# Optimization experiments

Measured on AMD Instinct MI355X. Metric: run time of the kernel, lower is better.

## Reference

```python
import jax, jax.numpy as jnp
import numpy as np

TOP_K = 2


def setup_inputs() -> dict:
    key = jax.random.key(0)
    ks = jax.random.split(key, 6)
    B, S, D, F, E = 4, 2048, 1024, 4096, 8
    sd = 1.0 / np.sqrt(D)
    sf = 1.0 / np.sqrt(F)
    return {
        "x": jax.random.normal(ks[0], (B, S, D), dtype=jnp.float32),
        "gate_w": jax.random.normal(ks[1], (D, E), dtype=jnp.float32) * sd,
        "w1": jax.random.normal(ks[2], (E, D, F), dtype=jnp.float32) * sd,
        "b1": jax.random.normal(ks[3], (E, F), dtype=jnp.float32) * 0.01,
        "w2": jax.random.normal(ks[4], (E, F, D), dtype=jnp.float32) * sf,
        "b2": jax.random.normal(ks[5], (E, D), dtype=jnp.float32) * 0.01,
    }


def reference(x, gate_w, w1, b1, w2, b2):
    B, S, D = x.shape
    E = gate_w.shape[1]
    xf = x.reshape(-1, D)                        # [T, D], T = B*S
    T = xf.shape[0]

    # Gating: top-k logits, softmax over the selected k (in fp32, as in torch)
    logits = xf @ gate_w                         # [T, E]
    top_vals, top_idx = jax.lax.top_k(logits, TOP_K)            # [T, K]
    wts = jax.nn.softmax(top_vals.astype(jnp.float32), axis=-1).astype(x.dtype)

    # Dense combine weights: combine[t, e] = sum_k wts[t,k] * [top_idx[t,k]==e]
    rows = jnp.arange(T)[:, None]
    combine = jnp.zeros((T, E), dtype=x.dtype).at[rows, top_idx].add(wts)

    # Expert FFNs (dropout is identity in eval; torch GELU default = exact erf)
    out = jnp.zeros_like(xf)
    for e in range(E):
        h = jax.nn.gelu(xf @ w1[e] + b1[e], approximate=False)  # [T, F]
        out = out + combine[:, e:e + 1] * (h @ w2[e] + b2[e])
    return out.reshape(B, S, D)
```

## Files before the change

### kernel.cpp

```cpp
#include <hip/hip_runtime.h>


#define T_TOK 8192
#define D_DIM 1024
#define F_DIM 4096
#define E_NUM 8
#define BM 128
#define BN 128
#define BK 32
#define NK1 (D_DIM / BK)
#define NK2 (F_DIM / BK)
#define MAX_TILES (T_TOK * 2 / BM + E_NUM)

typedef float f32x4 __attribute__((ext_vector_type(4)));
typedef short bf16x8 __attribute__((ext_vector_type(8)));

__device__ __forceinline__ unsigned short f2bf(float f) {
  union { float f; unsigned u; } v; v.f = f;
  unsigned r = v.u + 0x7FFFu + ((v.u >> 16) & 1u);
  return (unsigned short)(r >> 16);
}

__device__ __forceinline__ void async_cp16(const unsigned short* g, unsigned short* l) {
  __builtin_amdgcn_global_load_lds((__attribute__((address_space(1))) void*)g,
                                   (__attribute__((address_space(3))) void*)l,
                                   16, 0, 0);
}

#define WAIT_VM2 asm volatile("s_waitcnt vmcnt(2)" ::: "memory")
#define WAIT_LGKM0 asm volatile("s_waitcnt lgkmcnt(0)" ::: "memory")
#define RAW_BARRIER asm volatile("s_barrier" ::: "memory")


__global__ void cast_x_kernel(const float* __restrict__ src,
                              unsigned short* __restrict__ dst, int n4) {
  int i = blockIdx.x * blockDim.x + threadIdx.x;
  if (i >= n4) return;
  float4 v = ((const float4*)src)[i];
  ushort4 o;
  o.x = f2bf(v.x); o.y = f2bf(v.y); o.z = f2bf(v.z); o.w = f2bf(v.w);
  ((ushort4*)dst)[i] = o;
}

__global__ __launch_bounds__(256) void transpose_cast_kernel(
    const float* __restrict__ src, unsigned short* __restrict__ dst,
    int R, int C) {
  __shared__ float tile[64][65];
  int e = blockIdx.z;
  src += (size_t)e * R * C;
  dst += (size_t)e * R * C;
  int c0 = blockIdx.x * 64;
  int r0 = blockIdx.y * 64;
  int t = threadIdx.x;
  int cl = (t & 15) * 4, rl = t >> 4;
#pragma unroll
  for (int i = 0; i < 4; ++i) {
    int r = rl + i * 16;
    float4 v = *(const float4*)(src + (size_t)(r0 + r) * C + c0 + cl);
    tile[r][cl + 0] = v.x;
    tile[r][cl + 1] = v.y;
    tile[r][cl + 2] = v.z;
    tile[r][cl + 3] = v.w;
  }
  __syncthreads();
  int rl2 = (t & 15) * 4, cl2 = t >> 4;
#pragma unroll
  for (int i = 0; i < 4; ++i) {
    int c = cl2 + i * 16;
    ushort4 o;
    o.x = f2bf(tile[rl2 + 0][c]);
    o.y = f2bf(tile[rl2 + 1][c]);
    o.z = f2bf(tile[rl2 + 2][c]);
    o.w = f2bf(tile[rl2 + 3][c]);
    *(ushort4*)(dst + (size_t)(c0 + c) * R + r0 + rl2) = o;
  }
}

__global__ __launch_bounds__(256) void gate_kernel(
    const float* __restrict__ x, const float* __restrict__ gw,
    float* __restrict__ topk_w, int* __restrict__ topk_e) {
  int t = (blockIdx.x * 256 + threadIdx.x) >> 6;
  int lane = threadIdx.x & 63;
  const float* xr = x + (size_t)t * D_DIM;
  float acc[8];
#pragma unroll
  for (int e = 0; e < 8; ++e) acc[e] = 0.f;
  for (int j = 0; j < D_DIM / 64; ++j) {
    int d = lane + 64 * j;
    float xv = xr[d];
    float4 g0 = ((const float4*)(gw + (size_t)d * 8))[0];
    float4 g1 = ((const float4*)(gw + (size_t)d * 8))[1];
    acc[0] += xv * g0.x; acc[1] += xv * g0.y;
    acc[2] += xv * g0.z; acc[3] += xv * g0.w;
    acc[4] += xv * g1.x; acc[5] += xv * g1.y;
    acc[6] += xv * g1.z; acc[7] += xv * g1.w;
  }
#pragma unroll
  for (int off = 32; off > 0; off >>= 1) {
#pragma unroll
    for (int e = 0; e < 8; ++e) acc[e] += __shfl_xor(acc[e], off);
  }
  if (lane == 0) {
    int e0 = 0; float v0 = acc[0];
#pragma unroll
    for (int e = 1; e < 8; ++e)
      if (acc[e] > v0) { v0 = acc[e]; e0 = e; }
    int e1 = -1; float v1 = -1e30f;
#pragma unroll
    for (int e = 0; e < 8; ++e)
      if (e != e0 && acc[e] > v1) { v1 = acc[e]; e1 = e; }
    float ex = expf(v1 - v0);
    float inv = 1.f / (1.f + ex);
    topk_w[2 * t] = inv;
    topk_w[2 * t + 1] = ex * inv;
    topk_e[2 * t] = e0;
    topk_e[2 * t + 1] = e1;
  }
}

__global__ void scatter_kernel(const int* __restrict__ topk_e,
                               int* __restrict__ cnt, int* __restrict__ assign) {
  int idx = blockIdx.x * blockDim.x + threadIdx.x;
  int e = topk_e[idx];
  int pos = atomicAdd(&cnt[e], 1);
  assign[e * T_TOK + pos] = idx;
}

__global__ void tiles_kernel(const int* __restrict__ cnt,
                             int* __restrict__ ndesc, int4* __restrict__ desc) {
  if (threadIdx.x != 0) return;
  int nt = 0, hb = 0;
  for (int e = 0; e < E_NUM; ++e) {
    int c = cnt[e];
    for (int s = 0; s < c; s += BM) {
      int4 d;
      d.x = e; d.y = s; d.z = hb;
      d.w = (c - s < BM) ? (c - s) : BM;
      desc[nt++] = d;
    }
    hb += c;
  }
  *ndesc = nt;
}


__global__ __launch_bounds__(512, 6) void gemm1_kernel(
    const unsigned short* __restrict__ xb, const unsigned short* __restrict__ w1t,
    const float* __restrict__ b1, const int* __restrict__ assign,
    const int* __restrict__ ndesc, const int4* __restrict__ desc,
    unsigned short* __restrict__ H) {
  int tileid = blockIdx.y;
  if (tileid >= *ndesc) return;
  int4 dc = desc[tileid];
  int e = dc.x, start = dc.y, hbase = dc.z, mcnt = dc.w;
  int n0 = blockIdx.x * BN;

  __shared__ __attribute__((aligned(16))) unsigned short As[2][BM * BK];
  __shared__ __attribute__((aligned(16))) unsigned short Bs[2][BN * BK];

  int tid = threadIdx.x, lane = tid & 63, wv = tid >> 6;

  int row = tid >> 2, cc = tid & 3;
  int g = (cc - row) & 3;
  int rowc = row < mcnt ? row : (mcnt - 1);
  int a0 = assign[e * T_TOK + start + rowc];
  const unsigned short* gA = xb + (size_t)(a0 >> 1) * D_DIM + g * 8;
  const unsigned short* gB = w1t + (size_t)(e * F_DIM + n0 + row) * D_DIM + g * 8;
  int loff = wv * 512;

  int kc16 = lane >> 4, r16 = lane & 15;
  int m_off = (wv & 1) * 64, n_off = (wv >> 1) * 32;
  int aoff[4], boff[2];
#pragma unroll
  for (int i = 0; i < 4; ++i) {
    int ra = m_off + i * 16 + r16;
    aoff[i] = ra * 32 + ((kc16 + ra) & 3) * 8;
  }
#pragma unroll
  for (int j = 0; j < 2; ++j) {
    int rb = n_off + j * 16 + r16;
    boff[j] = rb * 32 + ((kc16 + rb) & 3) * 8;
  }

  f32x4 acc[4][2];
#pragma unroll
  for (int i = 0; i < 4; ++i)
#pragma unroll
    for (int j = 0; j < 2; ++j) acc[i][j] = (f32x4){0.f, 0.f, 0.f, 0.f};

  auto issue = [&](int t, int b) {
    int kc = (t < NK1 ? t : NK1 - 1) * BK;
    async_cp16(gA + kc, &As[b][loff]);
    async_cp16(gB + kc, &Bs[b][loff]);
  };
  auto step = [&](int kt, int b) {
    WAIT_VM2;
    RAW_BARRIER;
    bf16x8 af[4], bfr[2];
#pragma unroll
    for (int i = 0; i < 4; ++i) af[i] = *(const bf16x8*)(&As[b][0] + aoff[i]);
#pragma unroll
    for (int j = 0; j < 2; ++j) bfr[j] = *(const bf16x8*)(&Bs[b][0] + boff[j]);
    WAIT_LGKM0;
    RAW_BARRIER;
    issue(kt + 2, b);
#pragma unroll
    for (int i = 0; i < 4; ++i)
#pragma unroll
      for (int j = 0; j < 2; ++j)
        acc[i][j] = __builtin_amdgcn_mfma_f32_16x16x32_bf16(af[i], bfr[j], acc[i][j], 0, 0, 0);
  };

  issue(0, 0);
  issue(1, 1);
  for (int kt = 0; kt < NK1; kt += 2) { step(kt, 0); step(kt + 1, 1); }

  int col = lane & 15, rbase = (lane >> 4) * 4;
  float bias[2];
#pragma unroll
  for (int j = 0; j < 2; ++j) bias[j] = b1[e * F_DIM + n0 + n_off + j * 16 + col];
#pragma unroll
  for (int i = 0; i < 4; ++i) {
#pragma unroll
    for (int rg = 0; rg < 4; ++rg) {
      int r = m_off + i * 16 + rbase + rg;
      if (r < mcnt) {
        unsigned short* hrow = H + (size_t)(hbase + start + r) * F_DIM + n0 + n_off + col;
#pragma unroll
        for (int j = 0; j < 2; ++j) {
          float v = acc[i][j][rg] + bias[j];
          v = 0.5f * v * (1.0f + erff(v * 0.70710678118654752f));
          hrow[j * 16] = f2bf(v);
        }
      }
    }
  }
}

__global__ __launch_bounds__(512, 6) void gemm2_kernel(
    const unsigned short* __restrict__ H, const unsigned short* __restrict__ w2t,
    const float* __restrict__ b2, const int* __restrict__ assign,
    const float* __restrict__ topk_w,
    const int* __restrict__ ndesc, const int4* __restrict__ desc,
    float* __restrict__ out) {
  int tileid = blockIdx.y;
  if (tileid >= *ndesc) return;
  int4 dc = desc[tileid];
  int e = dc.x, start = dc.y, hbase = dc.z, mcnt = dc.w;
  int n0 = blockIdx.x * BN;

  __shared__ __attribute__((aligned(16))) unsigned short As[2][BM * BK];
  __shared__ __attribute__((aligned(16))) unsigned short Bs[2][BN * BK];

  int tid = threadIdx.x, lane = tid & 63, wv = tid >> 6;

  int row = tid >> 2, cc = tid & 3;
  int g = (cc - row) & 3;
  int rowc = row < mcnt ? row : (mcnt - 1);
  const unsigned short* gA = H + (size_t)(hbase + start + rowc) * F_DIM + g * 8;
  const unsigned short* gB = w2t + (size_t)(e * D_DIM + n0 + row) * F_DIM + g * 8;
  int loff = wv * 512;

  int kc16 = lane >> 4, r16 = lane & 15;
  int m_off = (wv & 1) * 64, n_off = (wv >> 1) * 32;
  int aoff[4], boff[2];
#pragma unroll
  for (int i = 0; i < 4; ++i) {
    int ra = m_off + i * 16 + r16;
    aoff[i] = ra * 32 + ((kc16 + ra) & 3) * 8;
  }
#pragma unroll
  for (int j = 0; j < 2; ++j) {
    int rb = n_off + j * 16 + r16;
    boff[j] = rb * 32 + ((kc16 + rb) & 3) * 8;
  }

  f32x4 acc[4][2];
#pragma unroll
  for (int i = 0; i < 4; ++i)
#pragma unroll
    for (int j = 0; j < 2; ++j) acc[i][j] = (f32x4){0.f, 0.f, 0.f, 0.f};

  auto issue = [&](int t, int b) {
    int kc = (t < NK2 ? t : NK2 - 1) * BK;
    async_cp16(gA + kc, &As[b][loff]);
    async_cp16(gB + kc, &Bs[b][loff]);
  };
  auto step = [&](int kt, int b) {
    WAIT_VM2;
    RAW_BARRIER;
    bf16x8 af[4], bfr[2];
#pragma unroll
    for (int i = 0; i < 4; ++i) af[i] = *(const bf16x8*)(&As[b][0] + aoff[i]);
#pragma unroll
    for (int j = 0; j < 2; ++j) bfr[j] = *(const bf16x8*)(&Bs[b][0] + boff[j]);
    WAIT_LGKM0;
    RAW_BARRIER;
    issue(kt + 2, b);
#pragma unroll
    for (int i = 0; i < 4; ++i)
#pragma unroll
      for (int j = 0; j < 2; ++j)
        acc[i][j] = __builtin_amdgcn_mfma_f32_16x16x32_bf16(af[i], bfr[j], acc[i][j], 0, 0, 0);
  };

  issue(0, 0);
  issue(1, 1);
  for (int kt = 0; kt < NK2; kt += 2) { step(kt, 0); step(kt + 1, 1); }

  int col = lane & 15, rbase = (lane >> 4) * 4;
  float bias[2];
#pragma unroll
  for (int j = 0; j < 2; ++j) bias[j] = b2[e * D_DIM + n0 + n_off + j * 16 + col];
#pragma unroll
  for (int i = 0; i < 4; ++i) {
#pragma unroll
    for (int rg = 0; rg < 4; ++rg) {
      int r = m_off + i * 16 + rbase + rg;
      if (r < mcnt) {
        int a = assign[e * T_TOK + start + r];
        float wt = topk_w[a];
        float* orow = out + (size_t)(a >> 1) * D_DIM + n0 + n_off + col;
#pragma unroll
        for (int j = 0; j < 2; ++j) {
          float v = acc[i][j][rg] + bias[j];
          atomicAdd(orow + j * 16, wt * v);
        }
      }
    }
  }
}


extern "C" void kernel_launch(void* const* d_in, const int* in_sizes, int n_in,
                              void* d_out, int out_size, void* d_ws, size_t ws_size,
                              hipStream_t stream) {
  const float* x      = (const float*)d_in[0];
  const float* gate_w = (const float*)d_in[1];
  const float* w1     = (const float*)d_in[2];
  const float* b1     = (const float*)d_in[3];
  const float* w2     = (const float*)d_in[4];
  const float* b2     = (const float*)d_in[5];
  float* out = (float*)d_out;

  char* ws = (char*)d_ws;
  size_t off = 0;
  auto alloc = [&](size_t bytes) {
    char* p = ws + off;
    off = (off + bytes + 255) & ~(size_t)255;
    return p;
  };
  unsigned short* xb   = (unsigned short*)alloc((size_t)T_TOK * D_DIM * 2);
  unsigned short* w1t  = (unsigned short*)alloc((size_t)E_NUM * D_DIM * F_DIM * 2);
  unsigned short* w2t  = (unsigned short*)alloc((size_t)E_NUM * D_DIM * F_DIM * 2);
  unsigned short* Hbuf = (unsigned short*)alloc((size_t)2 * T_TOK * F_DIM * 2);
  float* topk_w = (float*)alloc((size_t)2 * T_TOK * 4);
  int* topk_e   = (int*)alloc((size_t)2 * T_TOK * 4);
  int* assign   = (int*)alloc((size_t)E_NUM * T_TOK * 4);
  int* cnt      = (int*)alloc(64);
  int* ndesc    = (int*)alloc(64);
  int4* desc    = (int4*)alloc((size_t)MAX_TILES * 16);

  hipMemsetAsync(cnt, 0, 64, stream);
  hipMemsetAsync(out, 0, (size_t)out_size * 4, stream);

  cast_x_kernel<<<(T_TOK * D_DIM / 4 + 255) / 256, 256, 0, stream>>>(
      x, xb, T_TOK * D_DIM / 4);
  transpose_cast_kernel<<<dim3(F_DIM / 64, D_DIM / 64, E_NUM), 256, 0, stream>>>(
      w1, w1t, D_DIM, F_DIM);
  transpose_cast_kernel<<<dim3(D_DIM / 64, F_DIM / 64, E_NUM), 256, 0, stream>>>(
      w2, w2t, F_DIM, D_DIM);
  gate_kernel<<<T_TOK / 4, 256, 0, stream>>>(x, gate_w, topk_w, topk_e);
  scatter_kernel<<<2 * T_TOK / 256, 256, 0, stream>>>(topk_e, cnt, assign);
  tiles_kernel<<<1, 64, 0, stream>>>(cnt, ndesc, desc);
  gemm1_kernel<<<dim3(F_DIM / BN, MAX_TILES), 512, 0, stream>>>(
      xb, w1t, b1, assign, ndesc, desc, Hbuf);
  gemm2_kernel<<<dim3(D_DIM / BN, MAX_TILES), 512, 0, stream>>>(
      Hbuf, w2t, b2, assign, topk_w, ndesc, desc, out);
}
```

Measured before the change: 895.6 us.

## Enlarge MoE GEMM tiles to 256x256 and remap workgroups across XCDs

Doubles both tile dimensions of the two expert GEMMs. Each wave now computes a 128x64 sub-tile with 32 MFMA accumulators, and each thread issues two async loads per operand per k-step. The goal is more data reuse per LDS byte and fewer redundant global loads. A linear-to-XCD workgroup remapping is also added so consecutive tiles land on the same chiplet's L2. The costs are much higher register and LDS pressure (occupancy hint lowered to 2), more wasted work on partial expert tiles, and fewer workgroups to fill the GPU.

```diff
diff --git a/kernel.cpp b/kernel.cpp
--- a/kernel.cpp
+++ b/kernel.cpp
@@ -5,11 +5,13 @@
 #define D_DIM 1024
 #define F_DIM 4096
 #define E_NUM 8
-#define BM 128
-#define BN 128
+#define BM 256
+#define BN 256
 #define BK 32
 #define NK1 (D_DIM / BK)
 #define NK2 (F_DIM / BK)
+#define NX1 (F_DIM / BN)
+#define NX2 (D_DIM / BN)
 #define MAX_TILES (T_TOK * 2 / BM + E_NUM)
 
 typedef float f32x4 __attribute__((ext_vector_type(4)));
@@ -27,7 +29,7 @@
                                    16, 0, 0);
 }
 
-#define WAIT_VM2 asm volatile("s_waitcnt vmcnt(2)" ::: "memory")
+#define WAIT_VM4 asm volatile("s_waitcnt vmcnt(4)" ::: "memory")
 #define WAIT_LGKM0 asm volatile("s_waitcnt lgkmcnt(0)" ::: "memory")
 #define RAW_BARRIER asm volatile("s_barrier" ::: "memory")
 
@@ -144,16 +146,19 @@
 }
 
 
-__global__ __launch_bounds__(512, 6) void gemm1_kernel(
+__global__ __launch_bounds__(512, 2) void gemm1_kernel(
     const unsigned short* __restrict__ xb, const unsigned short* __restrict__ w1t,
     const float* __restrict__ b1, const int* __restrict__ assign,
     const int* __restrict__ ndesc, const int4* __restrict__ desc,
     unsigned short* __restrict__ H) {
-  int tileid = blockIdx.y;
+  const int nwg = NX1 * MAX_TILES;
+  int lin = blockIdx.y * NX1 + blockIdx.x;
+  int wg = (lin & 7) * (nwg >> 3) + (lin >> 3);
+  int tileid = wg / NX1;
+  int n0 = (wg & (NX1 - 1)) * BN;
   if (tileid >= *ndesc) return;
   int4 dc = desc[tileid];
   int e = dc.x, start = dc.y, hbase = dc.z, mcnt = dc.w;
-  int n0 = blockIdx.x * BN;
 
   __shared__ __attribute__((aligned(16))) unsigned short As[2][BM * BK];
   __shared__ __attribute__((aligned(16))) unsigned short Bs[2][BN * BK];
@@ -162,52 +167,59 @@
 
   int row = tid >> 2, cc = tid & 3;
   int g = (cc - row) & 3;
-  int rowc = row < mcnt ? row : (mcnt - 1);
-  int a0 = assign[e * T_TOK + start + rowc];
-  const unsigned short* gA = xb + (size_t)(a0 >> 1) * D_DIM + g * 8;
-  const unsigned short* gB = w1t + (size_t)(e * F_DIM + n0 + row) * D_DIM + g * 8;
+  int r1 = row + 128;
+  int r0c = row < mcnt ? row : (mcnt - 1);
+  int r1c = r1 < mcnt ? r1 : (mcnt - 1);
+  int a0 = assign[e * T_TOK + start + r0c];
+  int a1 = assign[e * T_TOK + start + r1c];
+  const unsigned short* gA0 = xb + (size_t)(a0 >> 1) * D_DIM + g * 8;
+  const unsigned short* gA1 = xb + (size_t)(a1 >> 1) * D_DIM + g * 8;
+  const unsigned short* gB0 = w1t + (size_t)(e * F_DIM + n0 + row) * D_DIM + g * 8;
+  const unsigned short* gB1 = w1t + (size_t)(e * F_DIM + n0 + r1) * D_DIM + g * 8;
   int loff = wv * 512;
 
   int kc16 = lane >> 4, r16 = lane & 15;
-  int m_off = (wv & 1) * 64, n_off = (wv >> 1) * 32;
-  int aoff[4], boff[2];
-#pragma unroll
-  for (int i = 0; i < 4; ++i) {
+  int m_off = (wv & 1) * 128, n_off = (wv >> 1) * 64;
+  int aoff[8], boff[4];
+#pragma unroll
+  for (int i = 0; i < 8; ++i) {
     int ra = m_off + i * 16 + r16;
     aoff[i] = ra * 32 + ((kc16 + ra) & 3) * 8;
   }
 #pragma unroll
-  for (int j = 0; j < 2; ++j) {
+  for (int j = 0; j < 4; ++j) {
     int rb = n_off + j * 16 + r16;
     boff[j] = rb * 32 + ((kc16 + rb) & 3) * 8;
   }
 
-  f32x4 acc[4][2];
-#pragma unroll
-  for (int i = 0; i < 4; ++i)
-#pragma unroll
-    for (int j = 0; j < 2; ++j) acc[i][j] = (f32x4){0.f, 0.f, 0.f, 0.f};
+  f32x4 acc[8][4];
+#pragma unroll
+  for (int i = 0; i < 8; ++i)
+#pragma unroll
+    for (int j = 0; j < 4; ++j) acc[i][j] = (f32x4){0.f, 0.f, 0.f, 0.f};
 
   auto issue = [&](int t, int b) {
     int kc = (t < NK1 ? t : NK1 - 1) * BK;
-    async_cp16(gA + kc, &As[b][loff]);
-    async_cp16(gB + kc, &Bs[b][loff]);
+    async_cp16(gA0 + kc, &As[b][loff]);
+    async_cp16(gA1 + kc, &As[b][loff + 4096]);
+    async_cp16(gB0 + kc, &Bs[b][loff]);
+    async_cp16(gB1 + kc, &Bs[b][loff + 4096]);
   };
   auto step = [&](int kt, int b) {
-    WAIT_VM2;
+    WAIT_VM4;
     RAW_BARRIER;
-    bf16x8 af[4], bfr[2];
-#pragma unroll
-    for (int i = 0; i < 4; ++i) af[i] = *(const bf16x8*)(&As[b][0] + aoff[i]);
-#pragma unroll
-    for (int j = 0; j < 2; ++j) bfr[j] = *(const bf16x8*)(&Bs[b][0] + boff[j]);
+    bf16x8 af[8], bfr[4];
+#pragma unroll
+    for (int i = 0; i < 8; ++i) af[i] = *(const bf16x8*)(&As[b][0] + aoff[i]);
+#pragma unroll
+    for (int j = 0; j < 4; ++j) bfr[j] = *(const bf16x8*)(&Bs[b][0] + boff[j]);
     WAIT_LGKM0;
     RAW_BARRIER;
     issue(kt + 2, b);
 #pragma unroll
-    for (int i = 0; i < 4; ++i)
-#pragma unroll
-      for (int j = 0; j < 2; ++j)
+    for (int i = 0; i < 8; ++i)
+#pragma unroll
+      for (int j = 0; j < 4; ++j)
         acc[i][j] = __builtin_amdgcn_mfma_f32_16x16x32_bf16(af[i], bfr[j], acc[i][j], 0, 0, 0);
   };
 
@@ -216,18 +228,18 @@
   for (int kt = 0; kt < NK1; kt += 2) { step(kt, 0); step(kt + 1, 1); }
 
   int col = lane & 15, rbase = (lane >> 4) * 4;
-  float bias[2];
-#pragma unroll
-  for (int j = 0; j < 2; ++j) bias[j] = b1[e * F_DIM + n0 + n_off + j * 16 + col];
-#pragma unroll
-  for (int i = 0; i < 4; ++i) {
+  float bias[4];
+#pragma unroll
+  for (int j = 0; j < 4; ++j) bias[j] = b1[e * F_DIM + n0 + n_off + j * 16 + col];
+#pragma unroll
+  for (int i = 0; i < 8; ++i) {
 #pragma unroll
     for (int rg = 0; rg < 4; ++rg) {
       int r = m_off + i * 16 + rbase + rg;
       if (r < mcnt) {
         unsigned short* hrow = H + (size_t)(hbase + start + r) * F_DIM + n0 + n_off + col;
 #pragma unroll
-        for (int j = 0; j < 2; ++j) {
+        for (int j = 0; j < 4; ++j) {
           float v = acc[i][j][rg] + bias[j];
           v = 0.5f * v * (1.0f + erff(v * 0.70710678118654752f));
           hrow[j * 16] = f2bf(v);
@@ -237,17 +249,20 @@
   }
 }
 
-__global__ __launch_bounds__(512, 6) void gemm2_kernel(
+__global__ __launch_bounds__(512, 2) void gemm2_kernel(
     const unsigned short* __restrict__ H, const unsigned short* __restrict__ w2t,
     const float* __restrict__ b2, const int* __restrict__ assign,
     const float* __restrict__ topk_w,
     const int* __restrict__ ndesc, const int4* __restrict__ desc,
     float* __restrict__ out) {
-  int tileid = blockIdx.y;
+  const int nwg = NX2 * MAX_TILES;
+  int lin = blockIdx.y * NX2 + blockIdx.x;
+  int wg = (lin & 7) * (nwg >> 3) + (lin >> 3);
+  int tileid = wg / NX2;
+  int n0 = (wg & (NX2 - 1)) * BN;
   if (tileid >= *ndesc) return;
   int4 dc = desc[tileid];
   int e = dc.x, start = dc.y, hbase = dc.z, mcnt = dc.w;
-  int n0 = blockIdx.x * BN;
 
   __shared__ __attribute__((aligned(16))) unsigned short As[2][BM * BK];
   __shared__ __attribute__((aligned(16))) unsigned short Bs[2][BN * BK];
@@ -256,51 +271,57 @@
 
   int row = tid >> 2, cc = tid & 3;
   int g = (cc - row) & 3;
-  int rowc = row < mcnt ? row : (mcnt - 1);
-  const unsigned short* gA = H + (size_t)(hbase + start + rowc) * F_DIM + g * 8;
-  const unsigned short* gB = w2t + (size_t)(e * D_DIM + n0 + row) * F_DIM + g * 8;
+  int r1 = row + 128;
+  int r0c = row < mcnt ? row : (mcnt - 1);
+  int r1c = r1 < mcnt ? r1 : (mcnt - 1);
+  const unsigned short* gA0 = H + (size_t)(hbase + start + r0c) * F_DIM + g * 8;
+  const unsigned short* gA1 = H + (size_t)(hbase + start + r1c) * F_DIM + g * 8;
+  const unsigned short* gB0 = w2t + (size_t)(e * D_DIM + n0 + row) * F_DIM + g * 8;
+  const unsigned short* gB1 = w2t + (size_t)(e * D_DIM + n0 + r1) * F_DIM + g * 8;
   int loff = wv * 512;
 
   int kc16 = lane >> 4, r16 = lane & 15;
-  int m_off = (wv & 1) * 64, n_off = (wv >> 1) * 32;
-  int aoff[4], boff[2];
-#pragma unroll
-  for (int i = 0; i < 4; ++i) {
+  int m_off = (wv & 1) * 128, n_off = (wv >> 1) * 64;
+  int aoff[8], boff[4];
+#pragma unroll
+  for (int i = 0; i < 8; ++i) {
     int ra = m_off + i * 16 + r16;
     aoff[i] = ra * 32 + ((kc16 + ra) & 3) * 8;
   }
 #pragma unroll
-  for (int j = 0; j < 2; ++j) {
+  for (int j = 0; j < 4; ++j) {
     int rb = n_off + j * 16 + r16;
     boff[j] = rb * 32 + ((kc16 + rb) & 3) * 8;
   }
 
-  f32x4 acc[4][2];
-#pragma unroll
-  for (int i = 0; i < 4; ++i)
-#pragma unroll
-    for (int j = 0; j < 2; ++j) acc[i][j] = (f32x4){0.f, 0.f, 0.f, 0.f};
+  f32x4 acc[8][4];
+#pragma unroll
+  for (int i = 0; i < 8; ++i)
+#pragma unroll
+    for (int j = 0; j < 4; ++j) acc[i][j] = (f32x4){0.f, 0.f, 0.f, 0.f};
 
   auto issue = [&](int t, int b) {
     int kc = (t < NK2 ? t : NK2 - 1) * BK;
-    async_cp16(gA + kc, &As[b][loff]);
-    async_cp16(gB + kc, &Bs[b][loff]);
+    async_cp16(gA0 + kc, &As[b][loff]);
+    async_cp16(gA1 + kc, &As[b][loff + 4096]);
+    async_cp16(gB0 + kc, &Bs[b][loff]);
+    async_cp16(gB1 + kc, &Bs[b][loff + 4096]);
   };
   auto step = [&](int kt, int b) {
-    WAIT_VM2;
+    WAIT_VM4;
     RAW_BARRIER;
-    bf16x8 af[4], bfr[2];
-#pragma unroll
-    for (int i = 0; i < 4; ++i) af[i] = *(const bf16x8*)(&As[b][0] + aoff[i]);
-#pragma unroll
-    for (int j = 0; j < 2; ++j) bfr[j] = *(const bf16x8*)(&Bs[b][0] + boff[j]);
+    bf16x8 af[8], bfr[4];
+#pragma unroll
+    for (int i = 0; i < 8; ++i) af[i] = *(const bf16x8*)(&As[b][0] + aoff[i]);
+#pragma unroll
+    for (int j = 0; j < 4; ++j) bfr[j] = *(const bf16x8*)(&Bs[b][0] + boff[j]);
     WAIT_LGKM0;
     RAW_BARRIER;
     issue(kt + 2, b);
 #pragma unroll
-    for (int i = 0; i < 4; ++i)
-#pragma unroll
-      for (int j = 0; j < 2; ++j)
+    for (int i = 0; i < 8; ++i)
+#pragma unroll
+      for (int j = 0; j < 4; ++j)
         acc[i][j] = __builtin_amdgcn_mfma_f32_16x16x32_bf16(af[i], bfr[j], acc[i][j], 0, 0, 0);
   };
 
@@ -309,11 +330,11 @@
   for (int kt = 0; kt < NK2; kt += 2) { step(kt, 0); step(kt + 1, 1); }
 
   int col = lane & 15, rbase = (lane >> 4) * 4;
-  float bias[2];
-#pragma unroll
-  for (int j = 0; j < 2; ++j) bias[j] = b2[e * D_DIM + n0 + n_off + j * 16 + col];
-#pragma unroll
-  for (int i = 0; i < 4; ++i) {
+  float bias[4];
+#pragma unroll
+  for (int j = 0; j < 4; ++j) bias[j] = b2[e * D_DIM + n0 + n_off + j * 16 + col];
+#pragma unroll
+  for (int i = 0; i < 8; ++i) {
 #pragma unroll
     for (int rg = 0; rg < 4; ++rg) {
       int r = m_off + i * 16 + rbase + rg;
@@ -322,7 +343,7 @@
         float wt = topk_w[a];
         float* orow = out + (size_t)(a >> 1) * D_DIM + n0 + n_off + col;
 #pragma unroll
-        for (int j = 0; j < 2; ++j) {
+        for (int j = 0; j < 4; ++j) {
           float v = acc[i][j][rg] + bias[j];
           atomicAdd(orow + j * 16, wt * v);
         }
@@ -373,8 +394,8 @@
   gate_kernel<<<T_TOK / 4, 256, 0, stream>>>(x, gate_w, topk_w, topk_e);
   scatter_kernel<<<2 * T_TOK / 256, 256, 0, stream>>>(topk_e, cnt, assign);
   tiles_kernel<<<1, 64, 0, stream>>>(cnt, ndesc, desc);
-  gemm1_kernel<<<dim3(F_DIM / BN, MAX_TILES), 512, 0, stream>>>(
+  gemm1_kernel<<<dim3(NX1, MAX_TILES), 512, 0, stream>>>(
       xb, w1t, b1, assign, ndesc, desc, Hbuf);
-  gemm2_kernel<<<dim3(D_DIM / BN, MAX_TILES), 512, 0, stream>>>(
+  gemm2_kernel<<<dim3(NX2, MAX_TILES), 512, 0, stream>>>(
       Hbuf, w2t, b2, assign, topk_w, ndesc, desc, out);
 }
```

New measurement: 1.002 ms. +11.8%, slower.
